# Kernel tuning notes

Hardware: AMD Instinct MI355X
Metric: run time of the kernel (lower is better)

Reference implementation:

```python
import jax, jax.numpy as jnp
import numpy as np

B, T, N, H, F, E = 8, 64, 2048, 64, 64, 32768
G = 3 * H  # GRU gate dim


def setup_inputs() -> dict:
    key = jax.random.key(0)
    ks = jax.random.split(key, 12)
    s = 0.05
    return {
        "x": jax.random.normal(ks[0], (B, T, N, F), jnp.float32),
        "targets": jax.random.normal(ks[1], (B, T, N, 1), jnp.float32),
        "targets_mask": jax.random.uniform(ks[2], (B, T, N, 1)) > 0.2,
        "edge_index": jax.random.randint(ks[3], (2, E), 0, N),
        "W_msg": jax.random.normal(ks[4], (H, H), jnp.float32) * s,
        "b_msg": jnp.zeros((H,), jnp.float32),
        "W_mix": jax.random.normal(ks[5], (H, H + F), jnp.float32) * s,
        "b_mix": jnp.zeros((H,), jnp.float32),
        "W_ih": jax.random.normal(ks[6], (N, G, H), jnp.float32) * s,
        "W_hh": jax.random.normal(ks[7], (N, G, H), jnp.float32) * s,
        "b_ih": jnp.zeros((N, G), jnp.float32),
        "b_hh": jnp.zeros((N, G), jnp.float32),
        "W_read": jax.random.normal(ks[8], (1, H), jnp.float32) * s,
        "b_read": jnp.zeros((1,), jnp.float32),
    }


def reference(x, targets, targets_mask, edge_index,
              W_msg, b_msg, W_mix, b_mix,
              W_ih, W_hh, b_ih, b_hh, W_read, b_read):
    src, dst = edge_index[0], edge_index[1]

    def step(state, x_t):
        # state: [B,N,H], x_t: [B,N,F]
        m = jnp.einsum('bnh,gh->bng', state, W_msg) + b_msg           # state_to_message
        agg = jnp.zeros_like(m).at[:, dst, :].add(m[:, src, :])       # add-aggregate over directed edges
        mi = jnp.concatenate([agg, x_t], axis=-1)                     # [B,N,H+F]
        m2 = jnp.einsum('bnf,hf->bnh', mi, W_mix) + b_mix             # mix_input
        # per-node independent GRU cells (batched weights [N,3H,*])
        gi = jnp.einsum('bnh,ngh->bng', m2, W_ih) + b_ih
        gh = jnp.einsum('bnh,ngh->bng', state, W_hh) + b_hh
        i_r, i_z, i_n = jnp.split(gi, 3, axis=-1)
        h_r, h_z, h_n = jnp.split(gh, 3, axis=-1)
        r = jax.nn.sigmoid(i_r + h_r)
        z = jax.nn.sigmoid(i_z + h_z)
        n_cand = jnp.tanh(i_n + r * h_n)
        new_state = (1.0 - z) * n_cand + z * state
        out = jnp.einsum('bnh,oh->bno', new_state, W_read) + b_read   # readout -> [B,N,1]
        return new_state, out

    state0 = jnp.zeros((B, N, H), x.dtype)
    _, outs = jax.lax.scan(step, state0, jnp.swapaxes(x, 0, 1))       # outs: [T,B,N,1]
    outputs = jnp.swapaxes(outs, 0, 1)                                # [B,T,N,1]
    loss = 0.5 * (outputs - targets) ** 2
    mask = targets_mask.astype(loss.dtype)
    return jnp.sum(loss * mask) / jnp.sum(mask)                       # masked mean
```

## Files before the change

kernel.cpp:

```cpp
#include <hip/hip_runtime.h>
#include <math.h>

namespace {
constexpr int B = 8, T = 64, N = 2048, H = 64, F = 64, E = 32768, G = 192;
constexpr int BNH = B * N * H;
constexpr int NWELEM = N * G * H;
constexpr int NBLK = 1024;
}

typedef __attribute__((ext_vector_type(8))) short bfrag;
typedef __attribute__((ext_vector_type(4))) float ffrag;
typedef long f8frag;

#define MFMA(a, b, c)  __builtin_amdgcn_mfma_f32_16x16x32_bf16(a, b, c, 0, 0, 0)
#define MFMA8(a, b, c) __builtin_amdgcn_mfma_f32_16x16x32_fp8_fp8(a, b, c, 0, 0, 0)

#define DS (1.f / 512.f)

__device__ __forceinline__ unsigned short f2bf(float f) {
  unsigned u = __float_as_uint(f);
  u += 0x7fffu + ((u >> 16) & 1u);
  return (unsigned short)(u >> 16);
}
__device__ __forceinline__ float bf2f(unsigned short u) {
  return __uint_as_float(((unsigned)u) << 16);
}
template<bool HI>
__device__ __forceinline__ unsigned cvtpk8(float a, float b, unsigned old) {
  return __builtin_amdgcn_cvt_pk_fp8_f32(a, b, old, HI);
}

__device__ __forceinline__ void grid_bar(int* bar, int t) {
  __syncthreads();
  if (threadIdx.x == 0) {
    __hip_atomic_fetch_add(&bar[(blockIdx.x & 63) * 16], 1,
                           __ATOMIC_RELEASE, __HIP_MEMORY_SCOPE_AGENT);
  }
  if (blockIdx.x == 0) {
    if (threadIdx.x < 64) {
      while (__hip_atomic_load(&bar[threadIdx.x * 16],
                               __ATOMIC_RELAXED, __HIP_MEMORY_SCOPE_AGENT) < 16 * (t + 1))
        __builtin_amdgcn_s_sleep(1);
      if (threadIdx.x == 0)
        __hip_atomic_store(&bar[4096], t + 1, __ATOMIC_RELAXED, __HIP_MEMORY_SCOPE_AGENT);
    }
  } else if (threadIdx.x == 0) {
    while (__hip_atomic_load(&bar[4096], __ATOMIC_RELAXED, __HIP_MEMORY_SCOPE_AGENT) < t + 1)
      __builtin_amdgcn_s_sleep(2);
  }
  __syncthreads();
}


__global__ __launch_bounds__(256) void init_kernel(
    float* __restrict__ state, unsigned short* __restrict__ mA,
    const float* __restrict__ b_msg, float* __restrict__ loss_acc,
    float* __restrict__ scal, int* __restrict__ deg, int* __restrict__ bar)
{
  int stride = gridDim.x * blockDim.x;
  for (int i = blockIdx.x * blockDim.x + threadIdx.x; i < BNH; i += stride) {
    state[i] = 0.f;
    mA[i] = f2bf(b_msg[i & (H - 1)]);
    if (i < 8192) bar[i] = 0;
    if (i < N) { loss_acc[i] = 0.f; deg[i] = 0; }
    if (i < 16) scal[i] = 0.f;
  }
}

__global__ __launch_bounds__(256) void conv_kernel(
    const float* __restrict__ Wi, const float* __restrict__ Wh,
    const float* __restrict__ Wm, const float* __restrict__ Wg,
    unsigned char* __restrict__ Wib, unsigned char* __restrict__ Whb,
    unsigned short* __restrict__ Wmb, unsigned short* __restrict__ Wgb)
{
  int stride = gridDim.x * blockDim.x * 2;
  for (int i = (blockIdx.x * blockDim.x + threadIdx.x) * 2; i < NWELEM; i += stride) {
    unsigned p = cvtpk8<false>(Wi[i] * 32.f, Wi[i + 1] * 32.f, 0u);
    *(unsigned short*)(Wib + i) = (unsigned short)p;
    p = cvtpk8<false>(Wh[i] * 32.f, Wh[i + 1] * 32.f, 0u);
    *(unsigned short*)(Whb + i) = (unsigned short)p;
    if (i < 64 * 128) { Wmb[i] = f2bf(Wm[i]); Wmb[i + 1] = f2bf(Wm[i + 1]); }
    if (i < 64 * 64)  { Wgb[i] = f2bf(Wg[i]); Wgb[i + 1] = f2bf(Wg[i + 1]); }
  }
}

__global__ __launch_bounds__(256) void hist_kernel(const int* __restrict__ ei, int* __restrict__ deg) {
  int e = blockIdx.x * 256 + threadIdx.x;
  if (e < E) atomicAdd(&deg[ei[E + e]], 1);
}

__global__ __launch_bounds__(1024) void scan_kernel(const int* __restrict__ deg,
    int* __restrict__ row_ptr, int* __restrict__ cursor)
{
  __shared__ int s[N];
  int tid = threadIdx.x;
  s[tid] = deg[tid];
  s[tid + 1024] = deg[tid + 1024];
  __syncthreads();
  for (int off = 1; off < N; off <<= 1) {
    int v0 = (tid >= off) ? s[tid - off] : 0;
    int v1 = s[tid + 1024 - off];
    __syncthreads();
    s[tid] += v0;
    s[tid + 1024] += v1;
    __syncthreads();
  }
  row_ptr[tid + 1] = s[tid];
  row_ptr[tid + 1025] = s[tid + 1024];
  cursor[tid] = (tid == 0) ? 0 : s[tid - 1];
  cursor[tid + 1024] = s[tid + 1023];
  if (tid == 0) row_ptr[0] = 0;
}

__global__ __launch_bounds__(256) void fill_kernel(const int* __restrict__ ei,
    int* __restrict__ cursor, int* __restrict__ col_src)
{
  int e = blockIdx.x * 256 + threadIdx.x;
  if (e < E) {
    int d = ei[E + e];
    int slot = atomicAdd(&cursor[d], 1);
    col_src[slot] = ei[e];
  }
}

__global__ __launch_bounds__(256) void mask_kernel(const int* __restrict__ mask, float* __restrict__ scal) {
  int stride = gridDim.x * blockDim.x;
  int v = 0;
  for (int i = blockIdx.x * blockDim.x + threadIdx.x; i < B * T * N; i += stride)
    v += (mask[i] != 0);
  for (int o = 1; o < 64; o <<= 1) v += __shfl_xor(v, o, 64);
  if ((threadIdx.x & 63) == 0) atomicAdd(&scal[0], (float)v);
}


__global__ __attribute__((amdgpu_flat_work_group_size(256, 256), amdgpu_waves_per_eu(4, 4)))
void persist_kernel(
    const float* __restrict__ x, const float* __restrict__ targets,
    const int* __restrict__ mask,
    const unsigned char* __restrict__ W_ihb, const unsigned char* __restrict__ W_hhb,
    const unsigned short* __restrict__ W_mixb, const unsigned short* __restrict__ W_msgb,
    const float* __restrict__ b_ih, const float* __restrict__ b_hh,
    const float* __restrict__ b_mix, const float* __restrict__ b_msg,
    const float* __restrict__ W_read, const float* __restrict__ b_read,
    const int* __restrict__ row_ptr, const int* __restrict__ col_src,
    unsigned short* __restrict__ mAb, unsigned short* __restrict__ mBb,
    float* __restrict__ loss_acc, int* __restrict__ bar)
{
  __shared__ float sts[2][8][64];
  __shared__ float partial[4][8][72];
  __shared__ unsigned char m2F8[8 * 80];
  __shared__ unsigned short nsA[8 * 72];
  __shared__ float redS[4][8];

  const int tid = threadIdx.x;
  const int w = tid >> 6, lane = tid & 63;
  const int mrow = lane & 15, quad = lane >> 4;
  const int n0 = blockIdx.x * 2;
  const bfrag za = (bfrag)0;
  const int hcol = w * 16 + mrow;

  f8frag whf[2][6], wif[2][6];
#pragma unroll
  for (int k = 0; k < 2; ++k) {
    const unsigned char* Wh = W_hhb + (size_t)(n0 + k) * (G * H);
    const unsigned char* Wi = W_ihb + (size_t)(n0 + k) * (G * H);
#pragma unroll
    for (int tt = 0; tt < 3; ++tt) {
      const int off = ((w + tt * 4) * 16 + mrow) * H + quad * 8;
      whf[k][2 * tt]     = *(const f8frag*)(Wh + off);
      whf[k][2 * tt + 1] = *(const f8frag*)(Wh + off + 32);
      wif[k][2 * tt]     = *(const f8frag*)(Wi + off);
      wif[k][2 * tt + 1] = *(const f8frag*)(Wi + off + 32);
    }
  }
  const unsigned short* wmp = W_mixb + hcol * 128 + quad * 8;
  const unsigned short* wgp = W_msgb + hcol * H + quad * 8;

  float bir[2], biz[2], bin_[2], bhr[2], bhz[2], bhn[2];
#pragma unroll
  for (int k = 0; k < 2; ++k) {
    const int bg = (n0 + k) * G + hcol;
    bir[k] = b_ih[bg]; biz[k] = b_ih[bg + 64]; bin_[k] = b_ih[bg + 128];
    bhr[k] = b_hh[bg]; bhz[k] = b_hh[bg + 64]; bhn[k] = b_hh[bg + 128];
  }
  float wrd = W_read[hcol];
  float bmix = b_mix[hcol];
  float bmsg = b_msg[hcol];
  const float brd = b_read[0];
  const int e0a = row_ptr[n0], e0b = row_ptr[n0 + 1], e0c = row_ptr[n0 + 2];

#pragma unroll
  for (int k = 0; k < 2; ++k) {
#pragma unroll
    for (int j = 0; j < 6; ++j) {
      asm volatile("" : "+v"(whf[k][j]));
      asm volatile("" : "+v"(wif[k][j]));
    }
    asm volatile("" : "+v"(bir[k]), "+v"(biz[k]), "+v"(bin_[k]),
                      "+v"(bhr[k]), "+v"(bhz[k]), "+v"(bhn[k]));
  }
  asm volatile("" : "+v"(wrd), "+v"(bmix), "+v"(bmsg));

  for (int i = tid; i < 2 * 8 * 64; i += 256) ((float*)sts)[i] = 0.f;
  __syncthreads();

  float lsum[2] = {0.f, 0.f};
  unsigned short* mcur = mAb;
  unsigned short* mnxt = mBb;

#pragma unroll 1
  for (int t = 0; t < T; ++t) {
#pragma unroll
    for (int k = 0; k < 2; ++k) {
      const int nn = n0 + k;
      const int ee0 = k ? e0b : e0a;
      const int ee1 = k ? e0c : e0b;

      bfrag wm0 = *(const bfrag*)(wmp);
      bfrag wm1 = *(const bfrag*)(wmp + 32);
      bfrag wm2 = *(const bfrag*)(wmp + 64);
      bfrag wm3 = *(const bfrag*)(wmp + 96);
      f8frag asF0 = 0, asF1 = 0;
      bfrag a2 = za, a3 = za;
      if (mrow < 8) {
        const float* sp = &sts[k][mrow][0];
        {
          float4 s0 = *(const float4*)(sp + quad * 8);
          float4 s1 = *(const float4*)(sp + quad * 8 + 4);
          unsigned u0 = 0, u1 = 0;
          u0 = cvtpk8<false>(s0.x * 16.f, s0.y * 16.f, u0);
          u0 = cvtpk8<true >(s0.z * 16.f, s0.w * 16.f, u0);
          u1 = cvtpk8<false>(s1.x * 16.f, s1.y * 16.f, u1);
          u1 = cvtpk8<true >(s1.z * 16.f, s1.w * 16.f, u1);
          asF0 = (f8frag)(((unsigned long long)u1 << 32) | u0);
          s0 = *(const float4*)(sp + 32 + quad * 8);
          s1 = *(const float4*)(sp + 32 + quad * 8 + 4);
          u0 = 0; u1 = 0;
          u0 = cvtpk8<false>(s0.x * 16.f, s0.y * 16.f, u0);
          u0 = cvtpk8<true >(s0.z * 16.f, s0.w * 16.f, u0);
          u1 = cvtpk8<false>(s1.x * 16.f, s1.y * 16.f, u1);
          u1 = cvtpk8<true >(s1.z * 16.f, s1.w * 16.f, u1);
          asF1 = (f8frag)(((unsigned long long)u1 << 32) | u0);
        }
        const float* xp = x + (((size_t)mrow * T + t) * N + nn) * F;
        {
          float4 t0 = *(const float4*)(xp + quad * 8);
          float4 t1 = *(const float4*)(xp + quad * 8 + 4);
          a2[0]=(short)f2bf(t0.x); a2[1]=(short)f2bf(t0.y); a2[2]=(short)f2bf(t0.z); a2[3]=(short)f2bf(t0.w);
          a2[4]=(short)f2bf(t1.x); a2[5]=(short)f2bf(t1.y); a2[6]=(short)f2bf(t1.z); a2[7]=(short)f2bf(t1.w);
          t0 = *(const float4*)(xp + 32 + quad * 8);
          t1 = *(const float4*)(xp + 32 + quad * 8 + 4);
          a3[0]=(short)f2bf(t0.x); a3[1]=(short)f2bf(t0.y); a3[2]=(short)f2bf(t0.z); a3[3]=(short)f2bf(t0.w);
          a3[4]=(short)f2bf(t1.x); a3[5]=(short)f2bf(t1.y); a3[6]=(short)f2bf(t1.z); a3[7]=(short)f2bf(t1.w);
        }
      }
      {
        float accL[4] = {0.f,0.f,0.f,0.f}, accH[4] = {0.f,0.f,0.f,0.f};
        const int j = lane & 31, bh = lane >> 5;
        const unsigned* mcU = (const unsigned*)mcur;
        for (int e = ee0 + w; e < ee1; e += 4) {
          const unsigned* mp = mcU + (size_t)col_src[e] * 256 + bh * 32 + j;
#pragma unroll
          for (int bb = 0; bb < 4; ++bb) {
            unsigned v = __hip_atomic_load(mp + bb * 64, __ATOMIC_RELAXED,
                                           __HIP_MEMORY_SCOPE_AGENT);
            accL[bb] += bf2f((unsigned short)(v & 0xffffu));
            accH[bb] += bf2f((unsigned short)(v >> 16));
          }
        }
#pragma unroll
        for (int bb = 0; bb < 4; ++bb) {
          partial[w][bb * 2 + bh][2 * j]     = accL[bb];
          partial[w][bb * 2 + bh][2 * j + 1] = accH[bb];
        }
      }
      ffrag ah0 = {0.f,0.f,0.f,0.f}, ah1 = {0.f,0.f,0.f,0.f}, ah2 = {0.f,0.f,0.f,0.f};
      ah0 = MFMA8(asF0, whf[k][0], ah0); ah0 = MFMA8(asF1, whf[k][1], ah0);
      ah1 = MFMA8(asF0, whf[k][2], ah1); ah1 = MFMA8(asF1, whf[k][3], ah1);
      ah2 = MFMA8(asF0, whf[k][4], ah2); ah2 = MFMA8(asF1, whf[k][5], ah2);
      __syncthreads();

      {
        bfrag a0 = za, a1 = za;
        if (mrow < 8) {
          const float* p = &partial[0][mrow][quad * 8];
#pragma unroll
          for (int j = 0; j < 8; ++j) {
            float s = p[j] + p[j + 576] + p[j + 1152] + p[j + 1728];
            a0[j] = (short)f2bf(s);
          }
          const float* p2 = &partial[0][mrow][32 + quad * 8];
#pragma unroll
          for (int j = 0; j < 8; ++j) {
            float s = p2[j] + p2[j + 576] + p2[j + 1152] + p2[j + 1728];
            a1[j] = (short)f2bf(s);
          }
        }
        ffrag accm = {0.f, 0.f, 0.f, 0.f};
        accm = MFMA(a0, wm0, accm);
        accm = MFMA(a1, wm1, accm);
        accm = MFMA(a2, wm2, accm);
        accm = MFMA(a3, wm3, accm);
        if (quad < 2) {
#pragma unroll
          for (int r = 0; r < 4; ++r) {
            unsigned p = cvtpk8<false>((accm[r] + bmix) * 16.f, 0.f, 0u);
            m2F8[(quad * 4 + r) * 80 + hcol] = (unsigned char)(p & 0xffu);
          }
        }
      }
      __syncthreads();

      bfrag wg0 = *(const bfrag*)(wgp);
      bfrag wg1 = *(const bfrag*)(wgp + 32);
      {
        f8frag amF0 = 0, amF1 = 0;
        if (mrow < 8) {
          amF0 = *(const f8frag*)&m2F8[mrow * 80 + quad * 8];
          amF1 = *(const f8frag*)&m2F8[mrow * 80 + 32 + quad * 8];
        }
        ffrag ai0 = {0.f,0.f,0.f,0.f}, ai1 = {0.f,0.f,0.f,0.f}, ai2 = {0.f,0.f,0.f,0.f};
        ai0 = MFMA8(amF0, wif[k][0], ai0); ai0 = MFMA8(amF1, wif[k][1], ai0);
        ai1 = MFMA8(amF0, wif[k][2], ai1); ai1 = MFMA8(amF1, wif[k][3], ai1);
        ai2 = MFMA8(amF0, wif[k][4], ai2); ai2 = MFMA8(amF1, wif[k][5], ai2);
        if (quad < 2) {
          float v[4];
#pragma unroll
          for (int r = 0; r < 4; ++r) {
            const int b = quad * 4 + r;
            float rs  = (ai0[r] + ah0[r]) * DS + bir[k] + bhr[k];
            float zs  = (ai1[r] + ah1[r]) * DS + biz[k] + bhz[k];
            float in_ = ai2[r] * DS + bin_[k];
            float hn  = ah2[r] * DS + bhn[k];
            float rg = 1.f / (1.f + __expf(-rs));
            float z  = 1.f / (1.f + __expf(-zs));
            float pre = in_ + rg * hn;
            float a = __expf(-2.f * fabsf(pre));
            float nc = copysignf((1.f - a) / (1.f + a), pre);
            float sold = sts[k][b][hcol];
            float ns = (1.f - z) * nc + z * sold;
            sts[k][b][hcol] = ns;
            nsA[b * 72 + hcol] = f2bf(ns);
            v[r] = ns * wrd;
          }
#pragma unroll
          for (int o = 1; o < 16; o <<= 1) {
#pragma unroll
            for (int r = 0; r < 4; ++r) v[r] += __shfl_xor(v[r], o, 64);
          }
          if (mrow == 0) {
#pragma unroll
            for (int r = 0; r < 4; ++r) redS[w][quad * 4 + r] = v[r];
          }
        }
      }
      __syncthreads();

      {
        bfrag an0 = za, an1 = za;
        if (mrow < 8) {
          an0 = *(const bfrag*)&nsA[mrow * 72 + quad * 8];
          an1 = *(const bfrag*)&nsA[mrow * 72 + 32 + quad * 8];
        }
        ffrag accg = {0.f, 0.f, 0.f, 0.f};
        accg = MFMA(an0, wg0, accg);
        accg = MFMA(an1, wg1, accg);
        if (quad < 2) {
          unsigned* mnU = (unsigned*)mnxt;
          const int jcol = hcol >> 1;
#pragma unroll
          for (int r = 0; r < 4; ++r) {
            float v0 = accg[r] + bmsg;
            float v1 = __shfl_xor(v0, 1, 64);
            if (!(mrow & 1)) {
              unsigned pk = (unsigned)f2bf(v0) | ((unsigned)f2bf(v1) << 16);
              __hip_atomic_store(&mnU[(size_t)nn * 256 + (quad * 4 + r) * 32 + jcol],
                                 pk, __ATOMIC_RELAXED, __HIP_MEMORY_SCOPE_AGENT);
            }
          }
        }
      }
      if (tid < 8) {
        float vv = redS[0][tid] + redS[1][tid] + redS[2][tid] + redS[3][tid] + brd;
        size_t idx = ((size_t)tid * T + t) * N + nn;
        float d = vv - targets[idx];
        float l = (mask[idx] != 0) ? 0.5f * d * d : 0.f;
        l += __shfl_xor(l, 1, 64);
        l += __shfl_xor(l, 2, 64);
        l += __shfl_xor(l, 4, 64);
        if (tid == 0) lsum[k] += l;
      }
    }
    grid_bar(bar, t);
    unsigned short* tp = mcur; mcur = mnxt; mnxt = tp;
  }
  if (tid == 0) { loss_acc[n0] = lsum[0]; loss_acc[n0 + 1] = lsum[1]; }
}


__global__ __launch_bounds__(256, 4) void step_kernel(
    const float* __restrict__ x, const float* __restrict__ targets,
    const int* __restrict__ mask, float* __restrict__ state,
    const unsigned char* __restrict__ W_ihb, const unsigned char* __restrict__ W_hhb,
    const unsigned short* __restrict__ W_mixb, const unsigned short* __restrict__ W_msgb,
    const float* __restrict__ b_ih, const float* __restrict__ b_hh,
    const float* __restrict__ b_mix, const float* __restrict__ b_msg,
    const float* __restrict__ W_read, const float* __restrict__ b_read,
    const int* __restrict__ row_ptr, const int* __restrict__ col_src,
    const unsigned short* __restrict__ m_cur, unsigned short* __restrict__ m_nxt,
    float* __restrict__ loss_acc, int t)
{
  __shared__ float partial[4][8][72];
  __shared__ unsigned char m2F8[8 * 80];
  __shared__ unsigned short nsA[8 * 72];
  __shared__ float redS[4][8];

  const int n = blockIdx.x;
  const int tid = threadIdx.x;
  const int w = tid >> 6, lane = tid & 63;
  const int mrow = lane & 15, quad = lane >> 4;
  const bfrag za = (bfrag)0;

  f8frag whf[6];
  {
    const unsigned char* Wh = W_hhb + (size_t)n * (G * H);
#pragma unroll
    for (int tt = 0; tt < 3; ++tt) {
      const unsigned char* wrh = Wh + (((w + tt * 4) * 16 + mrow) * H) + quad * 8;
      whf[2 * tt]     = *(const f8frag*)(wrh);
      whf[2 * tt + 1] = *(const f8frag*)(wrh + 32);
    }
  }
  f8frag asF0 = 0, asF1 = 0;
  float4 xv0 = {0.f,0.f,0.f,0.f}, xv1 = {0.f,0.f,0.f,0.f};
  float4 xv2 = {0.f,0.f,0.f,0.f}, xv3 = {0.f,0.f,0.f,0.f};
  if (mrow < 8) {
    const float* sp = state + (size_t)n * (B * H) + mrow * H;
    float4 s0 = *(const float4*)(sp + quad * 8);
    float4 s1 = *(const float4*)(sp + quad * 8 + 4);
    float4 s2 = *(const float4*)(sp + 32 + quad * 8);
    float4 s3 = *(const float4*)(sp + 32 + quad * 8 + 4);
    unsigned u0 = 0, u1 = 0;
    u0 = cvtpk8<false>(s0.x * 16.f, s0.y * 16.f, u0);
    u0 = cvtpk8<true >(s0.z * 16.f, s0.w * 16.f, u0);
    u1 = cvtpk8<false>(s1.x * 16.f, s1.y * 16.f, u1);
    u1 = cvtpk8<true >(s1.z * 16.f, s1.w * 16.f, u1);
    asF0 = (f8frag)(((unsigned long long)u1 << 32) | u0);
    u0 = 0; u1 = 0;
    u0 = cvtpk8<false>(s2.x * 16.f, s2.y * 16.f, u0);
    u0 = cvtpk8<true >(s2.z * 16.f, s2.w * 16.f, u0);
    u1 = cvtpk8<false>(s3.x * 16.f, s3.y * 16.f, u1);
    u1 = cvtpk8<true >(s3.z * 16.f, s3.w * 16.f, u1);
    asF1 = (f8frag)(((unsigned long long)u1 << 32) | u0);
    const float* xp = x + (((size_t)mrow * T + t) * N + n) * F;
    xv0 = *(const float4*)(xp + quad * 8);
    xv1 = *(const float4*)(xp + quad * 8 + 4);
    xv2 = *(const float4*)(xp + 32 + quad * 8);
    xv3 = *(const float4*)(xp + 32 + quad * 8 + 4);
  }
  {
    float acc[8] = {0.f,0.f,0.f,0.f,0.f,0.f,0.f,0.f};
    const int e0 = row_ptr[n], e1 = row_ptr[n + 1];
#pragma unroll 2
    for (int e = e0 + w; e < e1; e += 4) {
      const unsigned short* mp = m_cur + (size_t)col_src[e] * (B * H) + lane;
#pragma unroll
      for (int b = 0; b < 8; ++b) acc[b] += bf2f(mp[b * H]);
    }
#pragma unroll
    for (int b = 0; b < 8; ++b) partial[w][b][lane] = acc[b];
  }
  ffrag ah0 = {0.f,0.f,0.f,0.f}, ah1 = {0.f,0.f,0.f,0.f}, ah2 = {0.f,0.f,0.f,0.f};
  ah0 = MFMA8(asF0, whf[0], ah0); ah0 = MFMA8(asF1, whf[1], ah0);
  ah1 = MFMA8(asF0, whf[2], ah1); ah1 = MFMA8(asF1, whf[3], ah1);
  ah2 = MFMA8(asF0, whf[4], ah2); ah2 = MFMA8(asF1, whf[5], ah2);
  __syncthreads();

  f8frag wif[6];
  {
    const unsigned char* Wi = W_ihb + (size_t)n * (G * H);
#pragma unroll
    for (int tt = 0; tt < 3; ++tt) {
      const unsigned char* wri = Wi + (((w + tt * 4) * 16 + mrow) * H) + quad * 8;
      wif[2 * tt]     = *(const f8frag*)(wri);
      wif[2 * tt + 1] = *(const f8frag*)(wri + 32);
    }
  }
  {
    const int g0 = w * 16;
    bfrag a0 = za, a1 = za, a2 = za, a3 = za;
    if (mrow < 8) {
      const float* p = &partial[0][mrow][quad * 8];
#pragma unroll
      for (int j = 0; j < 8; ++j) {
        float s = p[j] + p[j + 576] + p[j + 1152] + p[j + 1728];
        a0[j] = (short)f2bf(s);
      }
      const float* p2 = &partial[0][mrow][32 + quad * 8];
#pragma unroll
      for (int j = 0; j < 8; ++j) {
        float s = p2[j] + p2[j + 576] + p2[j + 1152] + p2[j + 1728];
        a1[j] = (short)f2bf(s);
      }
      a2[0]=(short)f2bf(xv0.x); a2[1]=(short)f2bf(xv0.y); a2[2]=(short)f2bf(xv0.z); a2[3]=(short)f2bf(xv0.w);
      a2[4]=(short)f2bf(xv1.x); a2[5]=(short)f2bf(xv1.y); a2[6]=(short)f2bf(xv1.z); a2[7]=(short)f2bf(xv1.w);
      a3[0]=(short)f2bf(xv2.x); a3[1]=(short)f2bf(xv2.y); a3[2]=(short)f2bf(xv2.z); a3[3]=(short)f2bf(xv2.w);
      a3[4]=(short)f2bf(xv3.x); a3[5]=(short)f2bf(xv3.y); a3[6]=(short)f2bf(xv3.z); a3[7]=(short)f2bf(xv3.w);
    }
    const unsigned short* wm = W_mixb + (g0 + mrow) * 128 + quad * 8;
    ffrag accm = {0.f, 0.f, 0.f, 0.f};
    accm = MFMA(a0, *(const bfrag*)(wm), accm);
    accm = MFMA(a1, *(const bfrag*)(wm + 32), accm);
    accm = MFMA(a2, *(const bfrag*)(wm + 64), accm);
    accm = MFMA(a3, *(const bfrag*)(wm + 96), accm);
    if (quad < 2) {
      float bm = b_mix[g0 + mrow];
#pragma unroll
      for (int r = 0; r < 4; ++r) {
        unsigned p = cvtpk8<false>((accm[r] + bm) * 16.f, 0.f, 0u);
        m2F8[(quad * 4 + r) * 80 + g0 + mrow] = (unsigned char)(p & 0xffu);
      }
    }
  }
  __syncthreads();

  {
    f8frag amF0 = 0, amF1 = 0;
    if (mrow < 8) {
      amF0 = *(const f8frag*)&m2F8[mrow * 80 + quad * 8];
      amF1 = *(const f8frag*)&m2F8[mrow * 80 + 32 + quad * 8];
    }
    ffrag ai0 = {0.f,0.f,0.f,0.f}, ai1 = {0.f,0.f,0.f,0.f}, ai2 = {0.f,0.f,0.f,0.f};
    ai0 = MFMA8(amF0, wif[0], ai0); ai0 = MFMA8(amF1, wif[1], ai0);
    ai1 = MFMA8(amF0, wif[2], ai1); ai1 = MFMA8(amF1, wif[3], ai1);
    ai2 = MFMA8(amF0, wif[4], ai2); ai2 = MFMA8(amF1, wif[5], ai2);
    if (quad < 2) {
      const int hcol = w * 16 + mrow;
      const int bg = n * G + hcol;
      const float bir = b_ih[bg], biz = b_ih[bg + 64], bin_ = b_ih[bg + 128];
      const float bhr = b_hh[bg], bhz = b_hh[bg + 64], bhn = b_hh[bg + 128];
      const float wrd = W_read[hcol];
      float v[4];
#pragma unroll
      for (int r = 0; r < 4; ++r) {
        const int b = quad * 4 + r;
        float rs  = (ai0[r] + ah0[r]) * DS + bir + bhr;
        float zs  = (ai1[r] + ah1[r]) * DS + biz + bhz;
        float in_ = ai2[r] * DS + bin_;
        float hn  = ah2[r] * DS + bhn;
        float rg = 1.f / (1.f + __expf(-rs));
        float z  = 1.f / (1.f + __expf(-zs));
        float pre = in_ + rg * hn;
        float a = __expf(-2.f * fabsf(pre));
        float nc = copysignf((1.f - a) / (1.f + a), pre);
        float sold = state[(size_t)n * (B * H) + b * H + hcol];
        float ns = (1.f - z) * nc + z * sold;
        state[(size_t)n * (B * H) + b * H + hcol] = ns;
        nsA[b * 72 + hcol] = f2bf(ns);
        v[r] = ns * wrd;
      }
#pragma unroll
      for (int o = 1; o < 16; o <<= 1) {
#pragma unroll
        for (int r = 0; r < 4; ++r) v[r] += __shfl_xor(v[r], o, 64);
      }
      if (mrow == 0) {
#pragma unroll
        for (int r = 0; r < 4; ++r) redS[w][quad * 4 + r] = v[r];
      }
    }
  }
  __syncthreads();

  {
    const int g0 = w * 16;
    bfrag an0 = za, an1 = za;
    if (mrow < 8) {
      an0 = *(const bfrag*)&nsA[mrow * 72 + quad * 8];
      an1 = *(const bfrag*)&nsA[mrow * 72 + 32 + quad * 8];
    }
    const unsigned short* wg = W_msgb + (g0 + mrow) * H + quad * 8;
    ffrag accg = {0.f, 0.f, 0.f, 0.f};
    accg = MFMA(an0, *(const bfrag*)(wg), accg);
    accg = MFMA(an1, *(const bfrag*)(wg + 32), accg);
    if (quad < 2) {
      float bm = b_msg[g0 + mrow];
#pragma unroll
      for (int r = 0; r < 4; ++r)
        m_nxt[(size_t)n * (B * H) + (quad * 4 + r) * H + g0 + mrow] = f2bf(accg[r] + bm);
    }
  }
  if (tid < 8) {
    float vv = redS[0][tid] + redS[1][tid] + redS[2][tid] + redS[3][tid] + b_read[0];
    size_t idx = ((size_t)tid * T + t) * N + n;
    float d = vv - targets[idx];
    float l = (mask[idx] != 0) ? 0.5f * d * d : 0.f;
    l += __shfl_xor(l, 1, 64);
    l += __shfl_xor(l, 2, 64);
    l += __shfl_xor(l, 4, 64);
    if (tid == 0) loss_acc[n] += l;
  }
}

__global__ __launch_bounds__(256) void final_kernel(const float* __restrict__ loss_acc,
    const float* __restrict__ scal, float* __restrict__ out)
{
  __shared__ float sred[4];
  float v = 0.f;
  for (int i = threadIdx.x; i < N; i += 256) v += loss_acc[i];
  for (int o = 1; o < 64; o <<= 1) v += __shfl_xor(v, o, 64);
  if ((threadIdx.x & 63) == 0) sred[threadIdx.x >> 6] = v;
  __syncthreads();
  if (threadIdx.x == 0) out[0] = (sred[0] + sred[1] + sred[2] + sred[3]) / scal[0];
}

extern "C" void kernel_launch(void* const* d_in, const int* in_sizes, int n_in,
                              void* d_out, int out_size, void* d_ws, size_t ws_size,
                              hipStream_t stream)
{
  const float* x       = (const float*)d_in[0];
  const float* targets = (const float*)d_in[1];
  const int*   mask    = (const int*)d_in[2];
  const int*   ei      = (const int*)d_in[3];
  const float* W_msg   = (const float*)d_in[4];
  const float* b_msg   = (const float*)d_in[5];
  const float* W_mix   = (const float*)d_in[6];
  const float* b_mix   = (const float*)d_in[7];
  const float* W_ih    = (const float*)d_in[8];
  const float* W_hh    = (const float*)d_in[9];
  const float* b_ih    = (const float*)d_in[10];
  const float* b_hh    = (const float*)d_in[11];
  const float* W_read  = (const float*)d_in[12];
  const float* b_read  = (const float*)d_in[13];
  float* out = (float*)d_out;

  float* state          = (float*)d_ws;
  unsigned short* mA    = (unsigned short*)(state + BNH);
  unsigned short* mB    = mA + BNH;
  float* loss_acc       = (float*)(mB + BNH);
  float* scal           = loss_acc + N;
  int* deg              = (int*)(scal + 16);
  int* row_ptr          = deg + N;
  int* cursor           = row_ptr + (N + 16);
  int* col_src          = cursor + N;
  int* bar              = col_src + E;
  unsigned char* W_ihb  = (unsigned char*)(bar + 8192);
  unsigned char* W_hhb  = W_ihb + NWELEM;
  unsigned short* W_mixb = (unsigned short*)(W_hhb + NWELEM);
  unsigned short* W_msgb = W_mixb + 64 * 128;

  init_kernel<<<1024, 256, 0, stream>>>(state, mA, b_msg, loss_acc, scal, deg, bar);
  conv_kernel<<<8192, 256, 0, stream>>>(W_ih, W_hh, W_mix, W_msg, W_ihb, W_hhb, W_mixb, W_msgb);
  hist_kernel<<<E / 256, 256, 0, stream>>>(ei, deg);
  scan_kernel<<<1, 1024, 0, stream>>>(deg, row_ptr, cursor);
  fill_kernel<<<E / 256, 256, 0, stream>>>(ei, cursor, col_src);
  mask_kernel<<<512, 256, 0, stream>>>(mask, scal);

  int dev = 0, ncu = 0, occ = 0;
  hipGetDevice(&dev);
  hipDeviceGetAttribute(&ncu, hipDeviceAttributeMultiprocessorCount, dev);
  hipOccupancyMaxActiveBlocksPerMultiprocessor(&occ, (const void*)persist_kernel, 256, 0);
  const bool use_persist = ((long)occ * ncu >= NBLK);

  if (use_persist) {
    persist_kernel<<<NBLK, 256, 0, stream>>>(x, targets, mask,
                                             W_ihb, W_hhb, W_mixb, W_msgb,
                                             b_ih, b_hh, b_mix, b_msg, W_read, b_read,
                                             row_ptr, col_src, mA, mB, loss_acc, bar);
  } else {
    unsigned short* mcur = mA;
    unsigned short* mnxt = mB;
    for (int t = 0; t < T; ++t) {
      step_kernel<<<N, 256, 0, stream>>>(x, targets, mask, state,
                                         W_ihb, W_hhb, W_mixb, W_msgb,
                                         b_ih, b_hh, b_mix, b_msg, W_read, b_read,
                                         row_ptr, col_src, mcur, mnxt, loss_acc, t);
      unsigned short* tmp = mcur; mcur = mnxt; mnxt = tmp;
    }
  }
  final_kernel<<<1, 256, 0, stream>>>(loss_acc, scal, out);
}
```

Measured before the change: 2.221 ms.

## Use per-timestep message buffers to drop atomic loads and release fences

Replaces the two ping-pong message buffers with T+1 separate buffers, so each timestep writes to a fresh buffer. Neighbour messages can then be read with plain cached loads instead of agent-scope atomic loads, and the barrier's release atomic becomes relaxed. The non-persistent fallback path and the occupancy query are removed. The kernel no longer issues a release fence or reads with coherent atomics, so visibility of other blocks' writes across the grid barrier rests on stale cache lines never being present for fresh buffers. This risks correctness on hardware with non-coherent caches and needs much more workspace memory.

```diff
diff --git a/kernel.cpp b/kernel.cpp
--- a/kernel.cpp
+++ b/kernel.cpp
@@ -34,7 +34,7 @@
   __syncthreads();
   if (threadIdx.x == 0) {
     __hip_atomic_fetch_add(&bar[(blockIdx.x & 63) * 16], 1,
-                           __ATOMIC_RELEASE, __HIP_MEMORY_SCOPE_AGENT);
+                           __ATOMIC_RELAXED, __HIP_MEMORY_SCOPE_AGENT);
   }
   if (blockIdx.x == 0) {
     if (threadIdx.x < 64) {
@@ -48,19 +48,19 @@
     while (__hip_atomic_load(&bar[4096], __ATOMIC_RELAXED, __HIP_MEMORY_SCOPE_AGENT) < t + 1)
       __builtin_amdgcn_s_sleep(2);
   }
+  asm volatile("" ::: "memory");
   __syncthreads();
 }
 
 
 __global__ __launch_bounds__(256) void init_kernel(
-    float* __restrict__ state, unsigned short* __restrict__ mA,
-    const float* __restrict__ b_msg, float* __restrict__ loss_acc,
-    float* __restrict__ scal, int* __restrict__ deg, int* __restrict__ bar)
+    unsigned short* __restrict__ buf0, const float* __restrict__ b_msg,
+    float* __restrict__ loss_acc, float* __restrict__ scal,
+    int* __restrict__ deg, int* __restrict__ bar)
 {
   int stride = gridDim.x * blockDim.x;
   for (int i = blockIdx.x * blockDim.x + threadIdx.x; i < BNH; i += stride) {
-    state[i] = 0.f;
-    mA[i] = f2bf(b_msg[i & (H - 1)]);
+    buf0[i] = f2bf(b_msg[i & (H - 1)]);
     if (i < 8192) bar[i] = 0;
     if (i < N) { loss_acc[i] = 0.f; deg[i] = 0; }
     if (i < 16) scal[i] = 0.f;
@@ -143,7 +143,7 @@
     const float* __restrict__ b_mix, const float* __restrict__ b_msg,
     const float* __restrict__ W_read, const float* __restrict__ b_read,
     const int* __restrict__ row_ptr, const int* __restrict__ col_src,
-    unsigned short* __restrict__ mAb, unsigned short* __restrict__ mBb,
+    unsigned short* bufs,
     float* __restrict__ loss_acc, int* __restrict__ bar)
 {
   __shared__ float sts[2][8][64];
@@ -205,8 +205,8 @@
   __syncthreads();
 
   float lsum[2] = {0.f, 0.f};
-  unsigned short* mcur = mAb;
-  unsigned short* mnxt = mBb;
+  const unsigned short* mcur = bufs;
+  unsigned short* mnxt = bufs + BNH;
 
 #pragma unroll 1
   for (int t = 0; t < T; ++t) {
@@ -262,8 +262,7 @@
           const unsigned* mp = mcU + (size_t)col_src[e] * 256 + bh * 32 + j;
 #pragma unroll
           for (int bb = 0; bb < 4; ++bb) {
-            unsigned v = __hip_atomic_load(mp + bb * 64, __ATOMIC_RELAXED,
-                                           __HIP_MEMORY_SCOPE_AGENT);
+            unsigned v = mp[bb * 64];
             accL[bb] += bf2f((unsigned short)(v & 0xffffu));
             accH[bb] += bf2f((unsigned short)(v >> 16));
           }
@@ -392,214 +391,10 @@
       }
     }
     grid_bar(bar, t);
-    unsigned short* tp = mcur; mcur = mnxt; mnxt = tp;
+    mcur = mnxt;
+    mnxt += BNH;
   }
   if (tid == 0) { loss_acc[n0] = lsum[0]; loss_acc[n0 + 1] = lsum[1]; }
-}
-
-
-__global__ __launch_bounds__(256, 4) void step_kernel(
-    const float* __restrict__ x, const float* __restrict__ targets,
-    const int* __restrict__ mask, float* __restrict__ state,
-    const unsigned char* __restrict__ W_ihb, const unsigned char* __restrict__ W_hhb,
-    const unsigned short* __restrict__ W_mixb, const unsigned short* __restrict__ W_msgb,
-    const float* __restrict__ b_ih, const float* __restrict__ b_hh,
-    const float* __restrict__ b_mix, const float* __restrict__ b_msg,
-    const float* __restrict__ W_read, const float* __restrict__ b_read,
-    const int* __restrict__ row_ptr, const int* __restrict__ col_src,
-    const unsigned short* __restrict__ m_cur, unsigned short* __restrict__ m_nxt,
-    float* __restrict__ loss_acc, int t)
-{
-  __shared__ float partial[4][8][72];
-  __shared__ unsigned char m2F8[8 * 80];
-  __shared__ unsigned short nsA[8 * 72];
-  __shared__ float redS[4][8];
-
-  const int n = blockIdx.x;
-  const int tid = threadIdx.x;
-  const int w = tid >> 6, lane = tid & 63;
-  const int mrow = lane & 15, quad = lane >> 4;
-  const bfrag za = (bfrag)0;
-
-  f8frag whf[6];
-  {
-    const unsigned char* Wh = W_hhb + (size_t)n * (G * H);
-#pragma unroll
-    for (int tt = 0; tt < 3; ++tt) {
-      const unsigned char* wrh = Wh + (((w + tt * 4) * 16 + mrow) * H) + quad * 8;
-      whf[2 * tt]     = *(const f8frag*)(wrh);
-      whf[2 * tt + 1] = *(const f8frag*)(wrh + 32);
-    }
-  }
-  f8frag asF0 = 0, asF1 = 0;
-  float4 xv0 = {0.f,0.f,0.f,0.f}, xv1 = {0.f,0.f,0.f,0.f};
-  float4 xv2 = {0.f,0.f,0.f,0.f}, xv3 = {0.f,0.f,0.f,0.f};
-  if (mrow < 8) {
-    const float* sp = state + (size_t)n * (B * H) + mrow * H;
-    float4 s0 = *(const float4*)(sp + quad * 8);
-    float4 s1 = *(const float4*)(sp + quad * 8 + 4);
-    float4 s2 = *(const float4*)(sp + 32 + quad * 8);
-    float4 s3 = *(const float4*)(sp + 32 + quad * 8 + 4);
-    unsigned u0 = 0, u1 = 0;
-    u0 = cvtpk8<false>(s0.x * 16.f, s0.y * 16.f, u0);
-    u0 = cvtpk8<true >(s0.z * 16.f, s0.w * 16.f, u0);
-    u1 = cvtpk8<false>(s1.x * 16.f, s1.y * 16.f, u1);
-    u1 = cvtpk8<true >(s1.z * 16.f, s1.w * 16.f, u1);
-    asF0 = (f8frag)(((unsigned long long)u1 << 32) | u0);
-    u0 = 0; u1 = 0;
-    u0 = cvtpk8<false>(s2.x * 16.f, s2.y * 16.f, u0);
-    u0 = cvtpk8<true >(s2.z * 16.f, s2.w * 16.f, u0);
-    u1 = cvtpk8<false>(s3.x * 16.f, s3.y * 16.f, u1);
-    u1 = cvtpk8<true >(s3.z * 16.f, s3.w * 16.f, u1);
-    asF1 = (f8frag)(((unsigned long long)u1 << 32) | u0);
-    const float* xp = x + (((size_t)mrow * T + t) * N + n) * F;
-    xv0 = *(const float4*)(xp + quad * 8);
-    xv1 = *(const float4*)(xp + quad * 8 + 4);
-    xv2 = *(const float4*)(xp + 32 + quad * 8);
-    xv3 = *(const float4*)(xp + 32 + quad * 8 + 4);
-  }
-  {
-    float acc[8] = {0.f,0.f,0.f,0.f,0.f,0.f,0.f,0.f};
-    const int e0 = row_ptr[n], e1 = row_ptr[n + 1];
-#pragma unroll 2
-    for (int e = e0 + w; e < e1; e += 4) {
-      const unsigned short* mp = m_cur + (size_t)col_src[e] * (B * H) + lane;
-#pragma unroll
-      for (int b = 0; b < 8; ++b) acc[b] += bf2f(mp[b * H]);
-    }
-#pragma unroll
-    for (int b = 0; b < 8; ++b) partial[w][b][lane] = acc[b];
-  }
-  ffrag ah0 = {0.f,0.f,0.f,0.f}, ah1 = {0.f,0.f,0.f,0.f}, ah2 = {0.f,0.f,0.f,0.f};
-  ah0 = MFMA8(asF0, whf[0], ah0); ah0 = MFMA8(asF1, whf[1], ah0);
-  ah1 = MFMA8(asF0, whf[2], ah1); ah1 = MFMA8(asF1, whf[3], ah1);
-  ah2 = MFMA8(asF0, whf[4], ah2); ah2 = MFMA8(asF1, whf[5], ah2);
-  __syncthreads();
-
-  f8frag wif[6];
-  {
-    const unsigned char* Wi = W_ihb + (size_t)n * (G * H);
-#pragma unroll
-    for (int tt = 0; tt < 3; ++tt) {
-      const unsigned char* wri = Wi + (((w + tt * 4) * 16 + mrow) * H) + quad * 8;
-      wif[2 * tt]     = *(const f8frag*)(wri);
-      wif[2 * tt + 1] = *(const f8frag*)(wri + 32);
-    }
-  }
-  {
-    const int g0 = w * 16;
-    bfrag a0 = za, a1 = za, a2 = za, a3 = za;
-    if (mrow < 8) {
-      const float* p = &partial[0][mrow][quad * 8];
-#pragma unroll
-      for (int j = 0; j < 8; ++j) {
-        float s = p[j] + p[j + 576] + p[j + 1152] + p[j + 1728];
-        a0[j] = (short)f2bf(s);
-      }
-      const float* p2 = &partial[0][mrow][32 + quad * 8];
-#pragma unroll
-      for (int j = 0; j < 8; ++j) {
-        float s = p2[j] + p2[j + 576] + p2[j + 1152] + p2[j + 1728];
-        a1[j] = (short)f2bf(s);
-      }
-      a2[0]=(short)f2bf(xv0.x); a2[1]=(short)f2bf(xv0.y); a2[2]=(short)f2bf(xv0.z); a2[3]=(short)f2bf(xv0.w);
-      a2[4]=(short)f2bf(xv1.x); a2[5]=(short)f2bf(xv1.y); a2[6]=(short)f2bf(xv1.z); a2[7]=(short)f2bf(xv1.w);
-      a3[0]=(short)f2bf(xv2.x); a3[1]=(short)f2bf(xv2.y); a3[2]=(short)f2bf(xv2.z); a3[3]=(short)f2bf(xv2.w);
-      a3[4]=(short)f2bf(xv3.x); a3[5]=(short)f2bf(xv3.y); a3[6]=(short)f2bf(xv3.z); a3[7]=(short)f2bf(xv3.w);
-    }
-    const unsigned short* wm = W_mixb + (g0 + mrow) * 128 + quad * 8;
-    ffrag accm = {0.f, 0.f, 0.f, 0.f};
-    accm = MFMA(a0, *(const bfrag*)(wm), accm);
-    accm = MFMA(a1, *(const bfrag*)(wm + 32), accm);
-    accm = MFMA(a2, *(const bfrag*)(wm + 64), accm);
-    accm = MFMA(a3, *(const bfrag*)(wm + 96), accm);
-    if (quad < 2) {
-      float bm = b_mix[g0 + mrow];
-#pragma unroll
-      for (int r = 0; r < 4; ++r) {
-        unsigned p = cvtpk8<false>((accm[r] + bm) * 16.f, 0.f, 0u);
-        m2F8[(quad * 4 + r) * 80 + g0 + mrow] = (unsigned char)(p & 0xffu);
-      }
-    }
-  }
-  __syncthreads();
-
-  {
-    f8frag amF0 = 0, amF1 = 0;
-    if (mrow < 8) {
-      amF0 = *(const f8frag*)&m2F8[mrow * 80 + quad * 8];
-      amF1 = *(const f8frag*)&m2F8[mrow * 80 + 32 + quad * 8];
-    }
-    ffrag ai0 = {0.f,0.f,0.f,0.f}, ai1 = {0.f,0.f,0.f,0.f}, ai2 = {0.f,0.f,0.f,0.f};
-    ai0 = MFMA8(amF0, wif[0], ai0); ai0 = MFMA8(amF1, wif[1], ai0);
-    ai1 = MFMA8(amF0, wif[2], ai1); ai1 = MFMA8(amF1, wif[3], ai1);
-    ai2 = MFMA8(amF0, wif[4], ai2); ai2 = MFMA8(amF1, wif[5], ai2);
-    if (quad < 2) {
-      const int hcol = w * 16 + mrow;
-      const int bg = n * G + hcol;
-      const float bir = b_ih[bg], biz = b_ih[bg + 64], bin_ = b_ih[bg + 128];
-      const float bhr = b_hh[bg], bhz = b_hh[bg + 64], bhn = b_hh[bg + 128];
-      const float wrd = W_read[hcol];
-      float v[4];
-#pragma unroll
-      for (int r = 0; r < 4; ++r) {
-        const int b = quad * 4 + r;
-        float rs  = (ai0[r] + ah0[r]) * DS + bir + bhr;
-        float zs  = (ai1[r] + ah1[r]) * DS + biz + bhz;
-        float in_ = ai2[r] * DS + bin_;
-        float hn  = ah2[r] * DS + bhn;
-        float rg = 1.f / (1.f + __expf(-rs));
-        float z  = 1.f / (1.f + __expf(-zs));
-        float pre = in_ + rg * hn;
-        float a = __expf(-2.f * fabsf(pre));
-        float nc = copysignf((1.f - a) / (1.f + a), pre);
-        float sold = state[(size_t)n * (B * H) + b * H + hcol];
-        float ns = (1.f - z) * nc + z * sold;
-        state[(size_t)n * (B * H) + b * H + hcol] = ns;
-        nsA[b * 72 + hcol] = f2bf(ns);
-        v[r] = ns * wrd;
-      }
-#pragma unroll
-      for (int o = 1; o < 16; o <<= 1) {
-#pragma unroll
-        for (int r = 0; r < 4; ++r) v[r] += __shfl_xor(v[r], o, 64);
-      }
-      if (mrow == 0) {
-#pragma unroll
-        for (int r = 0; r < 4; ++r) redS[w][quad * 4 + r] = v[r];
-      }
-    }
-  }
-  __syncthreads();
-
-  {
-    const int g0 = w * 16;
-    bfrag an0 = za, an1 = za;
-    if (mrow < 8) {
-      an0 = *(const bfrag*)&nsA[mrow * 72 + quad * 8];
-      an1 = *(const bfrag*)&nsA[mrow * 72 + 32 + quad * 8];
-    }
-    const unsigned short* wg = W_msgb + (g0 + mrow) * H + quad * 8;
-    ffrag accg = {0.f, 0.f, 0.f, 0.f};
-    accg = MFMA(an0, *(const bfrag*)(wg), accg);
-    accg = MFMA(an1, *(const bfrag*)(wg + 32), accg);
-    if (quad < 2) {
-      float bm = b_msg[g0 + mrow];
-#pragma unroll
-      for (int r = 0; r < 4; ++r)
-        m_nxt[(size_t)n * (B * H) + (quad * 4 + r) * H + g0 + mrow] = f2bf(accg[r] + bm);
-    }
-  }
-  if (tid < 8) {
-    float vv = redS[0][tid] + redS[1][tid] + redS[2][tid] + redS[3][tid] + b_read[0];
-    size_t idx = ((size_t)tid * T + t) * N + n;
-    float d = vv - targets[idx];
-    float l = (mask[idx] != 0) ? 0.5f * d * d : 0.f;
-    l += __shfl_xor(l, 1, 64);
-    l += __shfl_xor(l, 2, 64);
-    l += __shfl_xor(l, 4, 64);
-    if (tid == 0) loss_acc[n] += l;
-  }
 }
 
 __global__ __launch_bounds__(256) void final_kernel(const float* __restrict__ loss_acc,
@@ -634,10 +429,8 @@
   const float* b_read  = (const float*)d_in[13];
   float* out = (float*)d_out;
 
-  float* state          = (float*)d_ws;
-  unsigned short* mA    = (unsigned short*)(state + BNH);
-  unsigned short* mB    = mA + BNH;
-  float* loss_acc       = (float*)(mB + BNH);
+  unsigned short* bufs  = (unsigned short*)d_ws;
+  float* loss_acc       = (float*)(bufs + (size_t)(T + 1) * BNH);
   float* scal           = loss_acc + N;
   int* deg              = (int*)(scal + 16);
   int* row_ptr          = deg + N;
@@ -649,34 +442,17 @@
   unsigned short* W_mixb = (unsigned short*)(W_hhb + NWELEM);
   unsigned short* W_msgb = W_mixb + 64 * 128;
 
-  init_kernel<<<1024, 256, 0, stream>>>(state, mA, b_msg, loss_acc, scal, deg, bar);
+  init_kernel<<<1024, 256, 0, stream>>>(bufs, b_msg, loss_acc, scal, deg, bar);
   conv_kernel<<<8192, 256, 0, stream>>>(W_ih, W_hh, W_mix, W_msg, W_ihb, W_hhb, W_mixb, W_msgb);
   hist_kernel<<<E / 256, 256, 0, stream>>>(ei, deg);
   scan_kernel<<<1, 1024, 0, stream>>>(deg, row_ptr, cursor);
   fill_kernel<<<E / 256, 256, 0, stream>>>(ei, cursor, col_src);
   mask_kernel<<<512, 256, 0, stream>>>(mask, scal);
 
-  int dev = 0, ncu = 0, occ = 0;
-  hipGetDevice(&dev);
-  hipDeviceGetAttribute(&ncu, hipDeviceAttributeMultiprocessorCount, dev);
-  hipOccupancyMaxActiveBlocksPerMultiprocessor(&occ, (const void*)persist_kernel, 256, 0);
-  const bool use_persist = ((long)occ * ncu >= NBLK);
-
-  if (use_persist) {
-    persist_kernel<<<NBLK, 256, 0, stream>>>(x, targets, mask,
-                                             W_ihb, W_hhb, W_mixb, W_msgb,
-                                             b_ih, b_hh, b_mix, b_msg, W_read, b_read,
-                                             row_ptr, col_src, mA, mB, loss_acc, bar);
-  } else {
-    unsigned short* mcur = mA;
-    unsigned short* mnxt = mB;
-    for (int t = 0; t < T; ++t) {
-      step_kernel<<<N, 256, 0, stream>>>(x, targets, mask, state,
-                                         W_ihb, W_hhb, W_mixb, W_msgb,
-                                         b_ih, b_hh, b_mix, b_msg, W_read, b_read,
-                                         row_ptr, col_src, mcur, mnxt, loss_acc, t);
-      unsigned short* tmp = mcur; mcur = mnxt; mnxt = tmp;
-    }
-  }
+  persist_kernel<<<NBLK, 256, 0, stream>>>(x, targets, mask,
+                                           W_ihb, W_hhb, W_mixb, W_msgb,
+                                           b_ih, b_hh, b_mix, b_msg, W_read, b_read,
+                                           row_ptr, col_src, bufs, loss_acc, bar);
+
   final_kernel<<<1, 256, 0, stream>>>(loss_acc, scal, out);
 }
```

New measurement: 2.180 ms, median of 2. About the same (-1.8%).
